# Kernel tuning notes

Measured on AMD Instinct MI355X. Metric: run time of the kernel, lower is better.

The kernel has to match this reference:

```python
import jax, jax.numpy as jnp
import numpy as np

F_FACETS = 400000
TEX_PER = 4            # textures per facet (counts sum must equal total textures)
T_TEX = F_FACETS * TEX_PER
C_IN = 64
C_OUT = 64
L = 2
N_BASIS = (L + 1) ** 2  # 9
BN_EPS = 1e-3


def setup_inputs() -> dict:
    key = jax.random.key(0)
    k1, k2, k3 = jax.random.split(key, 3)
    input_texture = jax.random.normal(k1, (T_TEX, C_IN), jnp.float32)
    bary_coeff = jax.random.uniform(k2, (T_TEX, N_BASIS), jnp.float32)
    # per-facet texture counts; constant 4 so counts sum exactly to T_TEX
    num_texture = jnp.full((F_FACETS,), TEX_PER, dtype=jnp.int32)
    # xavier_normal_ on [O, I, K]: fan_in = I*K, fan_out = ... torch uses fan_in=I*K? For 3D it treats dim1*rest.
    std = float(np.sqrt(2.0 / (C_IN * N_BASIS + C_OUT * N_BASIS)))
    weights = jax.random.normal(k3, (C_OUT, C_IN, N_BASIS), jnp.float32) * std
    biases = jnp.zeros((1, C_OUT), jnp.float32)
    gamma = jnp.ones((C_OUT,), jnp.float32)
    beta = jnp.zeros((C_OUT,), jnp.float32)
    return {
        "input_texture": input_texture,
        "bary_coeff": bary_coeff,
        "weights": weights,
        "biases": biases,
        "gamma": gamma,
        "beta": beta,
        "num_texture": num_texture,
    }


def reference(input_texture, bary_coeff, weights, biases, gamma, beta, num_texture):
    T = input_texture.shape[0]
    n_facets = num_texture.shape[0]
    n_basis = weights.shape[2]
    # per-texture contribution: contrib[t,o] = sum_{i,k} x[t,i] * W[o,i,k] * bary[t,k]
    # loop over small fixed basis count (9) to avoid a [T, I, K] intermediate
    contrib = jnp.zeros((T, weights.shape[0]), dtype=input_texture.dtype)
    for k in range(n_basis):
        contrib = contrib + (input_texture @ weights[:, :, k].T) * bary_coeff[:, k:k + 1]
    # scatter-sum per facet (ragged groups given by num_texture), then average
    seg_ids = jnp.repeat(jnp.arange(n_facets), num_texture, total_repeat_length=T)
    facet_sum = jax.ops.segment_sum(contrib, seg_ids, num_segments=n_facets)
    out = facet_sum / num_texture[:, None].astype(facet_sum.dtype)
    # bias + ReLU
    out = jax.nn.relu(out + biases)
    # BatchNorm1d in training mode: batch stats (biased variance), eps=1e-3
    mu = jnp.mean(out, axis=0)
    var = jnp.mean(jnp.square(out - mu), axis=0)
    out = (out - mu) * jax.lax.rsqrt(var + BN_EPS) * gamma + beta
    return out
```

## Files before the change

### kernel.cpp

```cpp
#include <hip/hip_runtime.h>


typedef _Float16 half8  __attribute__((ext_vector_type(8)));
typedef _Float16 h2     __attribute__((ext_vector_type(2)));
typedef __fp16   fp16x2 __attribute__((ext_vector_type(2)));
typedef float    f32x4  __attribute__((ext_vector_type(4)));

#define NGROUPS 100000
#define NPAIRS  50000
#define FFACETS 400000
#define GRID1   768
#define LDSP    9472

#define WAITV(N) asm volatile("s_waitcnt vmcnt(" #N ")" ::: "memory")
#define FENCE()  asm volatile("" ::: "memory")

union H8 { h2 h[4]; half8 v; };

static __device__ __forceinline__ h2 pkrtz(float a, float b) {
    fp16x2 r = __builtin_amdgcn_cvt_pkrtz(a, b);
    return __builtin_bit_cast(h2, r);
}

static __device__ __forceinline__ void gload16(const void* g, void* l) {
    __builtin_amdgcn_global_load_lds((const __attribute__((address_space(1))) void*)g,
                                     (__attribute__((address_space(3))) void*)l, 16, 0, 0);
}

__global__ __launch_bounds__(256) void prep_kernel(const float* __restrict__ W,
                                                   _Float16* __restrict__ wswz,
                                                   float* __restrict__ stats) {
    int idx = blockIdx.x * 256 + threadIdx.x;
    if (idx < 36864) {
        int j    = idx & 7;
        int lane = (idx >> 3) & 63;
        int mt   = (idx >> 9) & 3;
        int c    = idx >> 11;
        int o    = mt * 16 + (lane & 15);
        int i    = (c & 1) * 32 + ((lane >> 4) << 3) + j;
        int kb   = c >> 1;
        wswz[idx] = (_Float16)W[(o * 64 + i) * 9 + kb];
    }
    if (idx < 128) stats[idx] = 0.0f;
}

__global__ __launch_bounds__(256, 3) void pass1_kernel(
    const float* __restrict__ X, const float* __restrict__ BARY,
    const _Float16* __restrict__ WSWZ, const float* __restrict__ BIAS,
    const int* __restrict__ NTEX, float* __restrict__ OUT,
    float* __restrict__ stats) {

    __shared__ __align__(16) char ldsbuf[3 * LDSP];
    __shared__ float sl_s[64];
    __shared__ float sl_s2[64];

    const int tid  = threadIdx.x;
    const int wave = tid >> 6;
    const int lane = tid & 63;
    const int col  = lane & 15;
    const int quad = lane >> 4;

    half8 wf[18];
#pragma unroll
    for (int c = 0; c < 18; ++c)
        wf[c] = *(const half8*)(WSWZ + ((size_t)(c * 4 + wave) * 64 + lane) * 8);

    const f32x4 biasv = *(const f32x4*)(BIAS + wave * 16 + quad * 4);

    const int xdst = (wave << 10) + (lane << 4);
    const int xsrc = ((lane & 15) << 8) + ((lane >> 4) << 5)
                   + ((wave & 1) << 4) + ((wave >> 1) << 7);
    const char* Xb  = (const char*)X;
    const char* BAb = (const char*)BARY;
    const char* NTb = (const char*)NTEX;

    const int xrd = lane << 4;
    const int bco = 8192 + col * 36;
    const int nco = 9344 + ((col >> 2) << 2);

    float sacc[4]  = {0.f, 0.f, 0.f, 0.f};
    float s2acc[4] = {0.f, 0.f, 0.f, 0.f};

    const int b = blockIdx.x;
    const int n = (NPAIRS - 1 - b) / GRID1 + 1;

    auto STAGE = [&](char* S, int u) {
        const char* xs = Xb + (size_t)u * 8192;
        FENCE();
        gload16(xs + xsrc,        S + xdst);
        gload16(xs + 4096 + xsrc, S + 4096 + xdst);
        gload16(BAb + (size_t)u * 1152 + lane * 16, S + 8192 + lane * 16);
        if (lane < 8) gload16(BAb + (size_t)u * 1152 + 1024 + lane * 16, S + 9216 + lane * 16);
        if (lane < 2) gload16(NTb + (size_t)u * 32 + lane * 16,          S + 9344 + lane * 16);
        FENCE();
    };

    auto EPI = [&](f32x4 acc, float rc, int f) {
        f32x4 vv;
#pragma unroll
        for (int r = 0; r < 4; ++r) {
            float s = acc[r];
            s += __shfl_xor(s, 1);
            s += __shfl_xor(s, 2);
            s = s * rc + biasv[r];
            s = s > 0.f ? s : 0.f;
            vv[r] = s;
            sacc[r]  += s;
            s2acc[r] += s * s;
        }
        if ((col & 3) == 0)
            *(f32x4*)(OUT + (size_t)f * 64 + wave * 16 + quad * 4) = vv;
    };

    auto ITER = [&](const char* L, char* S, int u, int upre, bool do_stage) {
        __builtin_amdgcn_s_barrier();
        FENCE();
        f32x4 r0[4], r1[4];
#pragma unroll
        for (int j = 0; j < 4; ++j) {
            r0[j] = *(const f32x4*)(L + (j << 10) + xrd);
            r1[j] = *(const f32x4*)(L + 4096 + (j << 10) + xrd);
        }
        float bF0[9], bF1[9];
#pragma unroll
        for (int k = 0; k < 9; ++k) bF0[k] = *(const float*)(L + bco + k * 4);
#pragma unroll
        for (int k = 0; k < 9; ++k) bF1[k] = *(const float*)(L + bco + 576 + k * 4);
        const int nt0 = *(const int*)(L + nco);
        const int nt1 = *(const int*)(L + nco + 16);

        if (do_stage) STAGE(S, upre);

        h2 xh0[8], xh1[8], bh0[9], bh1[9];
        xh0[0] = pkrtz(r0[0][0], r0[0][1]);  xh0[1] = pkrtz(r0[0][2], r0[0][3]);
        xh0[2] = pkrtz(r0[1][0], r0[1][1]);  xh0[3] = pkrtz(r0[1][2], r0[1][3]);
        xh0[4] = pkrtz(r0[2][0], r0[2][1]);  xh0[5] = pkrtz(r0[2][2], r0[2][3]);
        xh0[6] = pkrtz(r0[3][0], r0[3][1]);  xh0[7] = pkrtz(r0[3][2], r0[3][3]);
        xh1[0] = pkrtz(r1[0][0], r1[0][1]);  xh1[1] = pkrtz(r1[0][2], r1[0][3]);
        xh1[2] = pkrtz(r1[1][0], r1[1][1]);  xh1[3] = pkrtz(r1[1][2], r1[1][3]);
        xh1[4] = pkrtz(r1[2][0], r1[2][1]);  xh1[5] = pkrtz(r1[2][2], r1[2][3]);
        xh1[6] = pkrtz(r1[3][0], r1[3][1]);  xh1[7] = pkrtz(r1[3][2], r1[3][3]);
#pragma unroll
        for (int k = 0; k < 9; ++k) { bh0[k] = pkrtz(bF0[k], bF0[k]); bh1[k] = pkrtz(bF1[k], bF1[k]); }
        const float rc0 = __builtin_amdgcn_rcpf((float)nt0);
        const float rc1 = __builtin_amdgcn_rcpf((float)nt1);

        f32x4 accA = {0.f, 0.f, 0.f, 0.f};
        f32x4 accB = {0.f, 0.f, 0.f, 0.f};
        __builtin_amdgcn_s_setprio(1);
#pragma unroll
        for (int c = 0; c < 18; ++c) {
            const int hh = (c & 1) * 4;
            const h2 bkA = bh0[c >> 1];
            const h2 bkB = bh1[c >> 1];
            H8 fa, fb;
            fa.h[0] = xh0[hh + 0] * bkA;  fa.h[1] = xh0[hh + 1] * bkA;
            fa.h[2] = xh0[hh + 2] * bkA;  fa.h[3] = xh0[hh + 3] * bkA;
            accA = __builtin_amdgcn_mfma_f32_16x16x32_f16(wf[c], fa.v, accA, 0, 0, 0);
            fb.h[0] = xh1[hh + 0] * bkB;  fb.h[1] = xh1[hh + 1] * bkB;
            fb.h[2] = xh1[hh + 2] * bkB;  fb.h[3] = xh1[hh + 3] * bkB;
            accB = __builtin_amdgcn_mfma_f32_16x16x32_f16(wf[c], fb.v, accB, 0, 0, 0);
        }
        __builtin_amdgcn_s_setprio(0);

        const int f0 = u * 8 + (col >> 2);
        EPI(accA, rc0, f0);
        EPI(accB, rc1, f0 + 4);
    };

    char* B0 = ldsbuf;
    char* B1 = ldsbuf + LDSP;
    char* B2 = ldsbuf + 2 * LDSP;

    STAGE(B0, b);
    STAGE(B1, b + GRID1);
    WAITV(5); ITER(B0, B2, b,         b + 2 * GRID1, true);
    WAITV(7); ITER(B1, B0, b + GRID1, b + 3 * GRID1, true);
    char *rd = B2, *st = B1, *ot = B0;
    int t = 2;
    for (; t < n - 2; ++t) {
        WAITV(9);
        ITER(rd, st, b + t * GRID1, b + (t + 2) * GRID1, true);
        char* tmp = ot; ot = st; st = rd; rd = tmp;
    }
    WAITV(9); ITER(rd, st, b + t * GRID1, 0, false);
    { char* tmp = ot; ot = st; st = rd; rd = tmp; } ++t;
    WAITV(4); ITER(rd, st, b + t * GRID1, 0, false);

#pragma unroll
    for (int r = 0; r < 4; ++r) {
        float s = sacc[r], s2 = s2acc[r];
        s  += __shfl_xor(s, 1);  s  += __shfl_xor(s, 2);
        s  += __shfl_xor(s, 4);  s  += __shfl_xor(s, 8);
        s2 += __shfl_xor(s2, 1); s2 += __shfl_xor(s2, 2);
        s2 += __shfl_xor(s2, 4); s2 += __shfl_xor(s2, 8);
        if (col == 0) {
            sl_s [wave * 16 + quad * 4 + r] = s  * 0.25f;
            sl_s2[wave * 16 + quad * 4 + r] = s2 * 0.25f;
        }
    }
    __syncthreads();
    if (tid < 64)        atomicAdd(&stats[tid],      sl_s [tid]);
    else if (tid < 128)  atomicAdd(&stats[tid],      sl_s2[tid - 64]);
}

__global__ __launch_bounds__(256) void pass3_kernel(float* __restrict__ OUT,
    const float* __restrict__ stats, const float* __restrict__ gamma,
    const float* __restrict__ beta) {
    const int tid = threadIdx.x;
    const size_t l = (size_t)blockIdx.x * 256 + tid;
    const int c0 = ((int)l & 15) * 4;
    float mu[4], sc[4], be[4];
    const float invF = 1.0f / (float)FFACETS;
#pragma unroll
    for (int u = 0; u < 4; ++u) {
        int ch = c0 + u;
        float m  = stats[ch] * invF;
        float va = stats[64 + ch] * invF - m * m;
        mu[u] = m;
        sc[u] = rsqrtf(va + 1e-3f) * gamma[ch];
        be[u] = beta[ch];
    }
    const size_t n4 = (size_t)FFACETS * 16;
    for (size_t i = l; i < n4; i += (size_t)gridDim.x * 256) {
        f32x4 v = ((f32x4*)OUT)[i];
#pragma unroll
        for (int u = 0; u < 4; ++u)
            v[u] = (v[u] - mu[u]) * sc[u] + be[u];
        ((f32x4*)OUT)[i] = v;
    }
}

extern "C" void kernel_launch(void* const* d_in, const int* in_sizes, int n_in,
                              void* d_out, int out_size, void* d_ws, size_t ws_size,
                              hipStream_t stream) {
    const float* X     = (const float*)d_in[0];
    const float* BARY  = (const float*)d_in[1];
    const float* W     = (const float*)d_in[2];
    const float* BIAS  = (const float*)d_in[3];
    const float* GAMMA = (const float*)d_in[4];
    const float* BETA  = (const float*)d_in[5];
    const int*   NTEX  = (const int*)d_in[6];
    float* OUT = (float*)d_out;

    _Float16* wswz = (_Float16*)d_ws;
    float* stats   = (float*)((char*)d_ws + 73728);

    prep_kernel<<<144, 256, 0, stream>>>(W, wswz, stats);
    pass1_kernel<<<GRID1, 256, 0, stream>>>(X, BARY, wswz, BIAS, NTEX, OUT, stats);
    pass3_kernel<<<2048, 256, 0, stream>>>(OUT, stats, GAMMA, BETA);
}
```

Before: 666.0 us.

## Fuse BatchNorm normalization into pass1 via grid-wide atomic barrier

Drops the separate pass3 launch. A device-wide spin barrier on an atomic counter in the workspace now runs at the end of pass1. After every block arrives, each block reads the global channel statistics and normalizes the output rows it wrote itself, which should still be in L2. This saves a kernel launch and may reduce DRAM traffic for the normalization pass. It relies on all 768 blocks being co-resident (256 CUs x 3 blocks) to avoid deadlock, and the counter is reset by prep_kernel.

```diff
diff --git a/kernel.cpp b/kernel.cpp
--- a/kernel.cpp
+++ b/kernel.cpp
@@ -5,6 +5,7 @@
 typedef _Float16 h2     __attribute__((ext_vector_type(2)));
 typedef __fp16   fp16x2 __attribute__((ext_vector_type(2)));
 typedef float    f32x4  __attribute__((ext_vector_type(4)));
+typedef float    f32x2  __attribute__((ext_vector_type(2)));
 
 #define NGROUPS 100000
 #define NPAIRS  50000
@@ -13,7 +14,9 @@
 #define LDSP    9472
 
 #define WAITV(N) asm volatile("s_waitcnt vmcnt(" #N ")" ::: "memory")
+#define WAITL0() asm volatile("s_waitcnt lgkmcnt(0)" ::: "memory")
 #define FENCE()  asm volatile("" ::: "memory")
+#define SB0()    __builtin_amdgcn_sched_barrier(0)
 
 union H8 { h2 h[4]; half8 v; };
 
@@ -41,14 +44,15 @@
         int kb   = c >> 1;
         wswz[idx] = (_Float16)W[(o * 64 + i) * 9 + kb];
     }
-    if (idx < 128) stats[idx] = 0.0f;
+    if (idx < 132) stats[idx] = 0.0f;
 }
 
 __global__ __launch_bounds__(256, 3) void pass1_kernel(
     const float* __restrict__ X, const float* __restrict__ BARY,
     const _Float16* __restrict__ WSWZ, const float* __restrict__ BIAS,
     const int* __restrict__ NTEX, float* __restrict__ OUT,
-    float* __restrict__ stats) {
+    float* __restrict__ stats, const float* __restrict__ GAMMA,
+    const float* __restrict__ BETA) {
 
     __shared__ __align__(16) char ldsbuf[3 * LDSP];
     __shared__ float sl_s[64];
@@ -202,32 +206,35 @@
     __syncthreads();
     if (tid < 64)        atomicAdd(&stats[tid],      sl_s [tid]);
     else if (tid < 128)  atomicAdd(&stats[tid],      sl_s2[tid - 64]);
-}
-
-__global__ __launch_bounds__(256) void pass3_kernel(float* __restrict__ OUT,
-    const float* __restrict__ stats, const float* __restrict__ gamma,
-    const float* __restrict__ beta) {
-    const int tid = threadIdx.x;
-    const size_t l = (size_t)blockIdx.x * 256 + tid;
-    const int c0 = ((int)l & 15) * 4;
-    float mu[4], sc[4], be[4];
+
+    int* done = (int*)(stats + 128);
+    WAITV(0);
+    __syncthreads();
+    if (tid == 0) {
+        __hip_atomic_fetch_add(done, 1, __ATOMIC_RELEASE, __HIP_MEMORY_SCOPE_AGENT);
+        int spins = 0;
+        while (__hip_atomic_load(done, __ATOMIC_ACQUIRE, __HIP_MEMORY_SCOPE_AGENT) < GRID1
+               && spins < (1 << 30)) { ++spins; __builtin_amdgcn_s_sleep(8); }
+    }
+    __syncthreads();
+
+    const int ch0 = (tid * 2) & 63;
     const float invF = 1.0f / (float)FFACETS;
-#pragma unroll
-    for (int u = 0; u < 4; ++u) {
-        int ch = c0 + u;
-        float m  = stats[ch] * invF;
-        float va = stats[64 + ch] * invF - m * m;
-        mu[u] = m;
-        sc[u] = rsqrtf(va + 1e-3f) * gamma[ch];
-        be[u] = beta[ch];
-    }
-    const size_t n4 = (size_t)FFACETS * 16;
-    for (size_t i = l; i < n4; i += (size_t)gridDim.x * 256) {
-        f32x4 v = ((f32x4*)OUT)[i];
-#pragma unroll
-        for (int u = 0; u < 4; ++u)
-            v[u] = (v[u] - mu[u]) * sc[u] + be[u];
-        ((f32x4*)OUT)[i] = v;
+    float s1a = __hip_atomic_load(&stats[ch0],          __ATOMIC_RELAXED, __HIP_MEMORY_SCOPE_AGENT);
+    float s2a = __hip_atomic_load(&stats[64 + ch0],     __ATOMIC_RELAXED, __HIP_MEMORY_SCOPE_AGENT);
+    float s1b = __hip_atomic_load(&stats[ch0 + 1],      __ATOMIC_RELAXED, __HIP_MEMORY_SCOPE_AGENT);
+    float s2b = __hip_atomic_load(&stats[64 + ch0 + 1], __ATOMIC_RELAXED, __HIP_MEMORY_SCOPE_AGENT);
+    const float mu0 = s1a * invF, va0 = s2a * invF - mu0 * mu0;
+    const float mu1 = s1b * invF, va1 = s2b * invF - mu1 * mu1;
+    const float sc0 = rsqrtf(va0 + 1e-3f) * GAMMA[ch0],     be0 = BETA[ch0];
+    const float sc1 = rsqrtf(va1 + 1e-3f) * GAMMA[ch0 + 1], be1 = BETA[ch0 + 1];
+
+    for (int u = b; u < NPAIRS; u += GRID1) {
+        float* p = OUT + (size_t)u * 512 + tid * 2;
+        f32x2 v = *(f32x2*)p;
+        v[0] = (v[0] - mu0) * sc0 + be0;
+        v[1] = (v[1] - mu1) * sc1 + be1;
+        *(f32x2*)p = v;
     }
 }
 
@@ -247,6 +254,5 @@
     float* stats   = (float*)((char*)d_ws + 73728);
 
     prep_kernel<<<144, 256, 0, stream>>>(W, wswz, stats);
-    pass1_kernel<<<GRID1, 256, 0, stream>>>(X, BARY, wswz, BIAS, NTEX, OUT, stats);
-    pass3_kernel<<<2048, 256, 0, stream>>>(OUT, stats, GAMMA, BETA);
-}
+    pass1_kernel<<<GRID1, 256, 0, stream>>>(X, BARY, wswz, BIAS, NTEX, OUT, stats, GAMMA, BETA);
+}
```

After: 795.5 us. 1.19x slower.

## Load X through registers, convert to fp16 and store swizzled LDS tiles

Applied to the files above, without the earlier changes.

Input texture rows stop going straight from global memory into LDS as fp32. Each wave now loads them into registers, converts them to packed fp16 and writes them into a smaller XOR-swizzled LDS buffer one iteration later. This halves the LDS footprint and read traffic per stage and drops the per-iteration fp32-to-fp16 conversion of the MFMA operands. In exchange it adds register-held prefetch state, extra vmcnt and lgkmcnt waits, and more complex pipeline bookkeeping that could expose load latency.

```diff
diff --git a/kernel.cpp b/kernel.cpp
--- a/kernel.cpp
+++ b/kernel.cpp
@@ -10,9 +10,10 @@
 #define NPAIRS  50000
 #define FFACETS 400000
 #define GRID1   768
-#define LDSP    9472
+#define LDSP    5280
 
 #define WAITV(N) asm volatile("s_waitcnt vmcnt(" #N ")" ::: "memory")
+#define WAITL0() asm volatile("s_waitcnt lgkmcnt(0)" ::: "memory")
 #define FENCE()  asm volatile("" ::: "memory")
 
 union H8 { h2 h[4]; half8 v; };
@@ -67,16 +68,17 @@
 
     const f32x4 biasv = *(const f32x4*)(BIAS + wave * 16 + quad * 4);
 
-    const int xdst = (wave << 10) + (lane << 4);
-    const int xsrc = ((lane & 15) << 8) + ((lane >> 4) << 5)
-                   + ((wave & 1) << 4) + ((wave >> 1) << 7);
+    const int xgsrc = (wave << 11) + (lane << 5);
+    const int xtex  = (wave << 3) + (lane >> 3);
+    const int xwr   = xtex * 128 + ((((lane & 7) ^ (xtex & 7))) << 4);
     const char* Xb  = (const char*)X;
     const char* BAb = (const char*)BARY;
     const char* NTb = (const char*)NTEX;
 
-    const int xrd = lane << 4;
-    const int bco = 8192 + col * 36;
-    const int nco = 9344 + ((col >> 2) << 2);
+    const int xr0 = (col << 7) + (((quad    ) ^ (col & 7)) << 4);
+    const int xr1 = (col << 7) + (((4 | quad) ^ (col & 7)) << 4);
+    const int bco = 4096 + col * 36;
+    const int nco = 5248 + ((col >> 2) << 2);
 
     float sacc[4]  = {0.f, 0.f, 0.f, 0.f};
     float s2acc[4] = {0.f, 0.f, 0.f, 0.f};
@@ -85,13 +87,27 @@
     const int n = (NPAIRS - 1 - b) / GRID1 + 1;
 
     auto STAGE = [&](char* S, int u) {
-        const char* xs = Xb + (size_t)u * 8192;
-        FENCE();
-        gload16(xs + xsrc,        S + xdst);
-        gload16(xs + 4096 + xsrc, S + 4096 + xdst);
-        gload16(BAb + (size_t)u * 1152 + lane * 16, S + 8192 + lane * 16);
-        if (lane < 8) gload16(BAb + (size_t)u * 1152 + 1024 + lane * 16, S + 9216 + lane * 16);
-        if (lane < 2) gload16(NTb + (size_t)u * 32 + lane * 16,          S + 9344 + lane * 16);
+        FENCE();
+        gload16(BAb + (size_t)u * 1152 + lane * 16, S + 4096 + lane * 16);
+        if (lane < 8) gload16(BAb + (size_t)u * 1152 + 1024 + lane * 16, S + 5120 + lane * 16);
+        if (lane < 2) gload16(NTb + (size_t)u * 32 + lane * 16,          S + 5248 + lane * 16);
+        FENCE();
+    };
+
+    auto XISSUE = [&](int u, f32x4& a, f32x4& b2) {
+        const char* xs = Xb + (size_t)u * 8192 + xgsrc;
+        FENCE();
+        a  = *(const f32x4*)(xs);
+        b2 = *(const f32x4*)(xs + 16);
+        FENCE();
+    };
+
+    auto XWRITE = [&](char* S, const f32x4& a, const f32x4& b2) {
+        H8 w;
+        w.h[0] = pkrtz(a[0],  a[1]);   w.h[1] = pkrtz(a[2],  a[3]);
+        w.h[2] = pkrtz(b2[0], b2[1]);  w.h[3] = pkrtz(b2[2], b2[3]);
+        FENCE();
+        *(half8*)(S + xwr) = w.v;
         FENCE();
     };
 
@@ -112,15 +128,15 @@
             *(f32x4*)(OUT + (size_t)f * 64 + wave * 16 + quad * 4) = vv;
     };
 
-    auto ITER = [&](const char* L, char* S, int u, int upre, bool do_stage) {
+    auto ITER = [&](const char* L, char* Sb, char* Sx, int u, int upre,
+                    bool do_issue, int midwait, bool do_write,
+                    f32x4& ca, f32x4& cb, f32x4& ia, f32x4& ib) {
         __builtin_amdgcn_s_barrier();
         FENCE();
-        f32x4 r0[4], r1[4];
-#pragma unroll
-        for (int j = 0; j < 4; ++j) {
-            r0[j] = *(const f32x4*)(L + (j << 10) + xrd);
-            r1[j] = *(const f32x4*)(L + 4096 + (j << 10) + xrd);
-        }
+        H8 e0 = *(const H8*)(L + xr0);
+        H8 o0 = *(const H8*)(L + xr1);
+        H8 e1 = *(const H8*)(L + 2048 + xr0);
+        H8 o1 = *(const H8*)(L + 2048 + xr1);
         float bF0[9], bF1[9];
 #pragma unroll
         for (int k = 0; k < 9; ++k) bF0[k] = *(const float*)(L + bco + k * 4);
@@ -129,17 +145,14 @@
         const int nt0 = *(const int*)(L + nco);
         const int nt1 = *(const int*)(L + nco + 16);
 
-        if (do_stage) STAGE(S, upre);
-
-        h2 xh0[8], xh1[8], bh0[9], bh1[9];
-        xh0[0] = pkrtz(r0[0][0], r0[0][1]);  xh0[1] = pkrtz(r0[0][2], r0[0][3]);
-        xh0[2] = pkrtz(r0[1][0], r0[1][1]);  xh0[3] = pkrtz(r0[1][2], r0[1][3]);
-        xh0[4] = pkrtz(r0[2][0], r0[2][1]);  xh0[5] = pkrtz(r0[2][2], r0[2][3]);
-        xh0[6] = pkrtz(r0[3][0], r0[3][1]);  xh0[7] = pkrtz(r0[3][2], r0[3][3]);
-        xh1[0] = pkrtz(r1[0][0], r1[0][1]);  xh1[1] = pkrtz(r1[0][2], r1[0][3]);
-        xh1[2] = pkrtz(r1[1][0], r1[1][1]);  xh1[3] = pkrtz(r1[1][2], r1[1][3]);
-        xh1[4] = pkrtz(r1[2][0], r1[2][1]);  xh1[5] = pkrtz(r1[2][2], r1[2][3]);
-        xh1[6] = pkrtz(r1[3][0], r1[3][1]);  xh1[7] = pkrtz(r1[3][2], r1[3][3]);
+        if (do_issue) { XISSUE(upre, ia, ib); STAGE(Sb, upre); }
+
+        if (do_write) {
+            if (midwait == 10) { WAITV(10); } else { WAITV(5); }
+            XWRITE(Sx, ca, cb);
+        }
+
+        h2 bh0[9], bh1[9];
 #pragma unroll
         for (int k = 0; k < 9; ++k) { bh0[k] = pkrtz(bF0[k], bF0[k]); bh1[k] = pkrtz(bF1[k], bF1[k]); }
         const float rc0 = __builtin_amdgcn_rcpf((float)nt0);
@@ -150,15 +163,16 @@
         __builtin_amdgcn_s_setprio(1);
 #pragma unroll
         for (int c = 0; c < 18; ++c) {
-            const int hh = (c & 1) * 4;
             const h2 bkA = bh0[c >> 1];
             const h2 bkB = bh1[c >> 1];
+            const H8& sA = (c & 1) ? o0 : e0;
+            const H8& sB = (c & 1) ? o1 : e1;
             H8 fa, fb;
-            fa.h[0] = xh0[hh + 0] * bkA;  fa.h[1] = xh0[hh + 1] * bkA;
-            fa.h[2] = xh0[hh + 2] * bkA;  fa.h[3] = xh0[hh + 3] * bkA;
+            fa.h[0] = sA.h[0] * bkA;  fa.h[1] = sA.h[1] * bkA;
+            fa.h[2] = sA.h[2] * bkA;  fa.h[3] = sA.h[3] * bkA;
             accA = __builtin_amdgcn_mfma_f32_16x16x32_f16(wf[c], fa.v, accA, 0, 0, 0);
-            fb.h[0] = xh1[hh + 0] * bkB;  fb.h[1] = xh1[hh + 1] * bkB;
-            fb.h[2] = xh1[hh + 2] * bkB;  fb.h[3] = xh1[hh + 3] * bkB;
+            fb.h[0] = sB.h[0] * bkB;  fb.h[1] = sB.h[1] * bkB;
+            fb.h[2] = sB.h[2] * bkB;  fb.h[3] = sB.h[3] * bkB;
             accB = __builtin_amdgcn_mfma_f32_16x16x32_f16(wf[c], fb.v, accB, 0, 0, 0);
         }
         __builtin_amdgcn_s_setprio(0);
@@ -166,26 +180,40 @@
         const int f0 = u * 8 + (col >> 2);
         EPI(accA, rc0, f0);
         EPI(accB, rc1, f0 + 4);
+        WAITL0();
     };
 
     char* B0 = ldsbuf;
     char* B1 = ldsbuf + LDSP;
     char* B2 = ldsbuf + 2 * LDSP;
 
-    STAGE(B0, b);
-    STAGE(B1, b + GRID1);
-    WAITV(5); ITER(B0, B2, b,         b + 2 * GRID1, true);
-    WAITV(7); ITER(B1, B0, b + GRID1, b + 3 * GRID1, true);
+    f32x4 xAa, xAb, xBa, xBb;
+    XISSUE(b, xAa, xAb);          STAGE(B0, b);
+    XISSUE(b + GRID1, xBa, xBb);  STAGE(B1, b + GRID1);
+    WAITV(0);
+    XWRITE(B0, xAa, xAb);
+    XWRITE(B1, xBa, xBb);
+    WAITL0();
+
+    ITER(B0, B2, B1, b, b + 2 * GRID1, true, 0, false, xBa, xBb, xAa, xAb);
+    ITER(B1, B0, B2, b + GRID1, b + 3 * GRID1, true, 10, true, xAa, xAb, xBa, xBb);
+
     char *rd = B2, *st = B1, *ot = B0;
     int t = 2;
     for (; t < n - 2; ++t) {
         WAITV(9);
-        ITER(rd, st, b + t * GRID1, b + (t + 2) * GRID1, true);
+        if (t & 1) ITER(rd, st, ot, b + t * GRID1, b + (t + 2) * GRID1, true, 10, true,
+                        xAa, xAb, xBa, xBb);
+        else       ITER(rd, st, ot, b + t * GRID1, b + (t + 2) * GRID1, true, 10, true,
+                        xBa, xBb, xAa, xAb);
         char* tmp = ot; ot = st; st = rd; rd = tmp;
     }
-    WAITV(9); ITER(rd, st, b + t * GRID1, 0, false);
+    WAITV(9);
+    if (t & 1) ITER(rd, st, ot, b + t * GRID1, 0, false, 5, true, xAa, xAb, xBa, xBb);
+    else       ITER(rd, st, ot, b + t * GRID1, 0, false, 5, true, xBa, xBb, xAa, xAb);
     { char* tmp = ot; ot = st; st = rd; rd = tmp; } ++t;
-    WAITV(4); ITER(rd, st, b + t * GRID1, 0, false);
+    WAITV(4);
+    ITER(rd, st, ot, b + t * GRID1, 0, false, 0, false, xAa, xAb, xBa, xBb);
 
 #pragma unroll
     for (int r = 0; r < 4; ++r) {
```

New measurement: 787.6 us. +18.3%, slower.
